# Kernel optimization log

Measured on AMD Instinct MI355X. Metric: run time of the kernel, lower is better.

## Reference

```python
import jax, jax.numpy as jnp
import numpy as np

D_MODEL = 2048
D_STATE = 128
D_CONV = 4
NHEADS = 64
NGROUPS = 1
HEAD_DIM = 64
CHUNK = 128
EPS = 1e-5
D_INNER = NHEADS * HEAD_DIM                       # 4096
CONV_DIM = D_INNER + 2 * NGROUPS * D_STATE        # 4352
D_IN_PROJ = 2 * D_INNER + 2 * NGROUPS * D_STATE + NHEADS  # 8512


def setup_inputs() -> dict:
    key = jax.random.key(0)
    ks = jax.random.split(key, 9)
    B, S = 2, 4096
    return dict(
        hidden_states=jax.random.normal(ks[0], (B, S, D_MODEL), jnp.float32),
        W_in=jax.random.normal(ks[1], (D_MODEL, D_IN_PROJ), jnp.float32) * 0.02,
        conv_w=jax.random.normal(ks[2], (CONV_DIM, D_CONV), jnp.float32) * 0.2,
        conv_b=jax.random.normal(ks[3], (CONV_DIM,), jnp.float32) * 0.1,
        # A must be negative (stable SSM): A = -exp(u), u ~ U[0,2)
        A=-jnp.exp(jax.random.uniform(ks[4], (NHEADS,), jnp.float32, 0.0, 2.0)),
        D=jax.random.normal(ks[5], (NHEADS,), jnp.float32),
        dt_bias=jax.random.normal(ks[6], (NHEADS,), jnp.float32),
        norm_w=jnp.ones((D_INNER,), jnp.float32),
        W_out=jax.random.normal(ks[7], (D_INNER, D_MODEL), jnp.float32) * 0.02,
    )


def _silu(x):
    return x * jax.nn.sigmoid(x)


def _causal_conv1d(x, w, b):
    # depthwise causal conv with silu; x [B,S,C], w [C,K], b [C]
    K = w.shape[1]
    S = x.shape[1]
    xp = jnp.pad(x, ((0, 0), (K - 1, 0), (0, 0)))
    y = sum(xp[:, k:k + S, :] * w[None, None, :, k].swapaxes(-1, -1) for k in range(0))
    y = jnp.zeros_like(x)
    for k in range(K):
        y = y + xp[:, k:k + S, :] * w[:, k][None, None, :]
    return _silu(y + b)


def _ssd(x, dt, A, Bm, Cm, chunk):
    # Mamba2 chunked SSD scan.
    # x [b,s,h,p]; dt [b,s,h] (>0); A [h]; Bm,Cm [b,s,g,n]
    b, s, h, p = x.shape
    g, n = Bm.shape[2], Bm.shape[3]
    hh = h // g
    c = s // chunk
    x = x.reshape(b, c, chunk, g, hh, p)
    dt = dt.reshape(b, c, chunk, g, hh)
    Bm = Bm.reshape(b, c, chunk, g, n)
    Cm = Cm.reshape(b, c, chunk, g, n)
    dA = dt * A.reshape(g, hh)                 # [b,c,l,g,hh]
    dA_cs = jnp.cumsum(dA, axis=2)             # [b,c,l,g,hh]
    dtx = dt[..., None] * x                    # [b,c,l,g,hh,p]
    # intra-chunk (diagonal blocks): L[i,j] = exp(sum_{j<k<=i} dA)
    diff = dA_cs[:, :, :, None] - dA_cs[:, :, None, :]   # [b,c,i,j,g,hh]
    mask = jnp.tril(jnp.ones((chunk, chunk), bool))
    L = jnp.exp(jnp.where(mask[None, None, :, :, None, None], diff, -jnp.inf))
    Y = jnp.einsum('bcign,bcjgn,bcijgh,bcjghp->bcighp', Cm, Bm, L, dtx)
    # chunk-final states
    decay = jnp.exp(dA_cs[:, :, -1:] - dA_cs)            # [b,c,l,g,hh]
    states = jnp.einsum('bcjgn,bcjgh,bcjghp->bcghpn', Bm, decay, dtx)
    chunk_decay = jnp.exp(dA_cs[:, :, -1])               # [b,c,g,hh]
    def step(prev, inp):
        cd, st = inp
        return cd[..., None, None] * prev + st, prev
    init = jnp.zeros_like(states[:, 0])
    _, prevs = jax.lax.scan(step, init,
                            (jnp.moveaxis(chunk_decay, 1, 0), jnp.moveaxis(states, 1, 0)))
    prevs = jnp.moveaxis(prevs, 0, 1)                    # [b,c,g,hh,p,n] state entering each chunk
    Y = Y + jnp.einsum('bcign,bcghpn,bcigh->bcighp', Cm, prevs, jnp.exp(dA_cs))
    return Y.reshape(b, s, h, p)


def reference(hidden_states, W_in, conv_w, conv_b, A, D, dt_bias, norm_w, W_out):
    Bsz, S, _ = hidden_states.shape
    zxbcdt = hidden_states @ W_in                        # [B,S,d_in_proj]
    z = zxbcdt[..., :D_INNER]
    xbc = zxbcdt[..., D_INNER:D_INNER + CONV_DIM]
    dt = zxbcdt[..., D_INNER + CONV_DIM:]                # [B,S,nheads]
    xbc = _causal_conv1d(xbc, conv_w, conv_b)            # silu-activated causal conv
    x = xbc[..., :D_INNER].reshape(Bsz, S, NHEADS, HEAD_DIM)
    Bm = xbc[..., D_INNER:D_INNER + NGROUPS * D_STATE].reshape(Bsz, S, NGROUPS, D_STATE)
    Cm = xbc[..., D_INNER + NGROUPS * D_STATE:].reshape(Bsz, S, NGROUPS, D_STATE)
    dt = jax.nn.softplus(dt + dt_bias)                   # delta_softplus, dt_limit=(0,inf)
    y = _ssd(x, dt, A, Bm, Cm, CHUNK)
    y = y + D[None, None, :, None] * x                   # skip (D) term
    y = y.reshape(Bsz, S, D_INNER)
    # gated RMSNorm (norm_before_gate=False): normalize(y * silu(z)), grouped
    yg = y * _silu(z)
    gsz = D_INNER // NGROUPS
    ygr = yg.reshape(Bsz, S, NGROUPS, gsz)
    rms = jax.lax.rsqrt(jnp.mean(ygr * ygr, axis=-1, keepdims=True) + EPS)
    yn = (ygr * rms).reshape(Bsz, S, D_INNER) * norm_w
    return yn @ W_out
```

## Files before the change

kernel.cpp:

```cpp
#include <hip/hip_runtime.h>
#include <hip/hip_bf16.h>

typedef __bf16 bf16_t;
typedef bf16_t bf16x8 __attribute__((ext_vector_type(8)));
typedef float f32x4 __attribute__((ext_vector_type(4)));

#define TOK 8192
#define DMODEL 2048
#define DINNER 4096
#define XBCN 4352
#define DSTATE 128
#define NH 64
#define HD 64
#define NBC 64
#define WINT_ROWS 8448

__device__ __forceinline__ void gld16(const bf16_t* g, bf16_t* l) {
  __builtin_amdgcn_global_load_lds((const __attribute__((address_space(1))) void*)g,
                                   (__attribute__((address_space(3))) void*)l, 16, 0, 0);
}

__device__ __forceinline__ f32x4 mfma16(bf16x8 a, bf16x8 b, f32x4 c) {
  return __builtin_amdgcn_mfma_f32_16x16x32_bf16(a, b, c, 0, 0, 0);
}


__global__ __launch_bounds__(256)
void cast_split_kernel(const float* __restrict__ in, bf16_t* __restrict__ hi,
                       bf16_t* __restrict__ lo, size_t n) {
  size_t i = ((size_t)blockIdx.x * 256 + threadIdx.x) * 8;
  if (i + 8 > n) return;
  float4 a = *(const float4*)(in + i);
  float4 b = *(const float4*)(in + i + 4);
  float v[8] = {a.x,a.y,a.z,a.w,b.x,b.y,b.z,b.w};
  bf16x8 h, l;
#pragma unroll
  for (int j = 0; j < 8; ++j) {
    h[j] = (bf16_t)v[j];
    l[j] = (bf16_t)(v[j] - (float)h[j]);
  }
  *(bf16x8*)(hi + i) = h;
  *(bf16x8*)(lo + i) = l;
}

__global__ __launch_bounds__(256)
void transpose_cast_kernel(const float* __restrict__ in, bf16_t* __restrict__ out,
                           int R, int C, int outRows) {
  __shared__ float tile[32][33];
  const int c0 = blockIdx.x * 32;
  const int r0 = blockIdx.y * 32;
  const int tx = threadIdx.x & 31;
  const int ty = threadIdx.x >> 5;
#pragma unroll
  for (int k = 0; k < 4; ++k) {
    int r = r0 + ty + k*8;
    int c = c0 + tx;
    tile[ty + k*8][tx] = (c < C) ? in[(size_t)r * C + c] : 0.f;
  }
  __syncthreads();
#pragma unroll
  for (int k = 0; k < 4; ++k) {
    int oc = c0 + ty + k*8;
    int orr = r0 + tx;
    out[(size_t)oc * R + orr] = (bf16_t)tile[tx][ty + k*8];
  }
}

__global__ __launch_bounds__(256)
void wdt_split_kernel(const float* __restrict__ Win, bf16_t* __restrict__ Whi,
                      bf16_t* __restrict__ Wlo) {
  const int h = threadIdx.x & 63;
  const int k0 = blockIdx.x * 256 + (threadIdx.x >> 6) * 64;
#pragma unroll 4
  for (int i = 0; i < 64; ++i) {
    int k = k0 + i;
    float v = Win[(size_t)k * 8512 + 8448 + h];
    bf16_t hv = (bf16_t)v;
    Whi[(size_t)h * DMODEL + k] = hv;
    Wlo[(size_t)h * DMODEL + k] = (bf16_t)(v - (float)hv);
  }
}

template <typename OutT>
__global__ __launch_bounds__(512, 2)
void gemm256(const bf16_t* __restrict__ A, const bf16_t* __restrict__ B,
             OutT* __restrict__ C0, OutT* __restrict__ C1,
             long M, long N, long K, long splitN, int gridX) {
  __shared__ bf16_t sA[2][2][8192];
  __shared__ bf16_t sB[2][2][8192];
  const int tid = threadIdx.x;
  const int lane = tid & 63;
  const int wid = tid >> 6;
  const int wr = wid >> 2;
  const int wc = wid & 3;

  const int nwg = gridDim.x;
  const int cpx = nwg >> 3;
  const int swz = (blockIdx.x & 7) * cpx + (blockIdx.x >> 3);
  const long bm = (long)(swz / gridX) * 256;
  const long bn = (long)(swz % gridX) * 256;

  const int srow = (wid >> 1) * 16 + (lane & 15);
  const int skof = (wid & 1) * 32 + (lane >> 4) * 8;
  const bf16_t* Abase = A + (bm + srow) * K + skof;
  const bf16_t* Bbase = B + (bn + srow) * K + skof;

  auto stageA = [&](int buf, int h, long kt) {
    const bf16_t* s = Abase + (long)h * 128 * K + kt;
    gld16(s,          &sA[buf][h][wid * 512]);
    gld16(s + 64 * K, &sA[buf][h][4096 + wid * 512]);
  };
  auto stageB = [&](int buf, int h, long kt) {
    const bf16_t* s = Bbase + (long)h * 128 * K + kt;
    gld16(s,          &sB[buf][h][wid * 512]);
    gld16(s + 64 * K, &sB[buf][h][4096 + wid * 512]);
  };
  auto rdA = [&](int buf, int h, int f, int s) -> bf16x8 {
    return *(const bf16x8*)&sA[buf][h][((f * 2 + s) * 64 + lane) * 8];
  };
  auto rdB = [&](int buf, int h, int f, int s) -> bf16x8 {
    return *(const bf16x8*)&sB[buf][h][((f * 2 + s) * 64 + lane) * 8];
  };

  stageA(0, 0, 0); stageB(0, 0, 0); stageB(0, 1, 0); stageA(0, 1, 0);

  f32x4 acc[8][4] = {};
  bf16x8 a[4][2], b[2][2];
  int cur = 0;
  const int NT = (int)(K >> 6);

  for (int t = 0; t < NT; ++t) {
    const bool fin = (t == NT - 1);
    const long ktn = (long)(t + 1) * 64;
    asm volatile("s_waitcnt vmcnt(4)\n\ts_barrier" ::: "memory");
#pragma unroll
    for (int mi = 0; mi < 4; ++mi) {
      a[mi][0] = rdA(cur, 0, wr*4 + mi, 0);
      a[mi][1] = rdA(cur, 0, wr*4 + mi, 1);
    }
#pragma unroll
    for (int ni = 0; ni < 2; ++ni) {
      b[ni][0] = rdB(cur, 0, wc*2 + ni, 0);
      b[ni][1] = rdB(cur, 0, wc*2 + ni, 1);
    }
    if (!fin) stageA(cur ^ 1, 0, ktn);
    __builtin_amdgcn_s_setprio(1);
#pragma unroll
    for (int mi = 0; mi < 4; ++mi)
#pragma unroll
      for (int ni = 0; ni < 2; ++ni) {
        acc[mi][ni] = mfma16(a[mi][0], b[ni][0], acc[mi][ni]);
        acc[mi][ni] = mfma16(a[mi][1], b[ni][1], acc[mi][ni]);
      }
    __builtin_amdgcn_s_setprio(0);
    if (!fin) asm volatile("s_waitcnt vmcnt(4)\n\ts_barrier" ::: "memory");
    else      asm volatile("s_waitcnt vmcnt(2)\n\ts_barrier" ::: "memory");
#pragma unroll
    for (int ni = 0; ni < 2; ++ni) {
      b[ni][0] = rdB(cur, 1, wc*2 + ni, 0);
      b[ni][1] = rdB(cur, 1, wc*2 + ni, 1);
    }
    if (!fin) stageB(cur ^ 1, 0, ktn);
    __builtin_amdgcn_s_setprio(1);
#pragma unroll
    for (int mi = 0; mi < 4; ++mi)
#pragma unroll
      for (int ni = 0; ni < 2; ++ni) {
        acc[mi][2 + ni] = mfma16(a[mi][0], b[ni][0], acc[mi][2 + ni]);
        acc[mi][2 + ni] = mfma16(a[mi][1], b[ni][1], acc[mi][2 + ni]);
      }
    __builtin_amdgcn_s_setprio(0);
    if (!fin) asm volatile("s_waitcnt vmcnt(4)\n\ts_barrier" ::: "memory");
    else      asm volatile("s_waitcnt vmcnt(0)\n\ts_barrier" ::: "memory");
#pragma unroll
    for (int mi = 0; mi < 4; ++mi) {
      a[mi][0] = rdA(cur, 1, wr*4 + mi, 0);
      a[mi][1] = rdA(cur, 1, wr*4 + mi, 1);
    }
    if (!fin) stageB(cur ^ 1, 1, ktn);
    __builtin_amdgcn_s_setprio(1);
#pragma unroll
    for (int mi = 0; mi < 4; ++mi)
#pragma unroll
      for (int ni = 0; ni < 2; ++ni) {
        acc[4 + mi][2 + ni] = mfma16(a[mi][0], b[ni][0], acc[4 + mi][2 + ni]);
        acc[4 + mi][2 + ni] = mfma16(a[mi][1], b[ni][1], acc[4 + mi][2 + ni]);
      }
    __builtin_amdgcn_s_setprio(0);
    asm volatile("s_barrier" ::: "memory");
#pragma unroll
    for (int ni = 0; ni < 2; ++ni) {
      b[ni][0] = rdB(cur, 0, wc*2 + ni, 0);
      b[ni][1] = rdB(cur, 0, wc*2 + ni, 1);
    }
    if (!fin) stageA(cur ^ 1, 1, ktn);
    __builtin_amdgcn_s_setprio(1);
#pragma unroll
    for (int mi = 0; mi < 4; ++mi)
#pragma unroll
      for (int ni = 0; ni < 2; ++ni) {
        acc[4 + mi][ni] = mfma16(a[mi][0], b[ni][0], acc[4 + mi][ni]);
        acc[4 + mi][ni] = mfma16(a[mi][1], b[ni][1], acc[4 + mi][ni]);
      }
    __builtin_amdgcn_s_setprio(0);
    cur ^= 1;
  }

  const int cr = (lane >> 4) * 4;
  const int cc = lane & 15;
  OutT* Cb;
  long col0, ldc;
  if (bn < splitN) { Cb = C0; col0 = bn; ldc = splitN; }
  else             { Cb = C1; col0 = bn - splitN; ldc = N - splitN; }
#pragma unroll
  for (int mi = 0; mi < 8; ++mi) {
    long row = bm + (mi >> 2) * 128 + wr * 64 + (mi & 3) * 16 + cr;
#pragma unroll
    for (int ni = 0; ni < 4; ++ni) {
      long col = col0 + (ni >> 1) * 128 + wc * 32 + (ni & 1) * 16 + cc;
      OutT* p = Cb + row * ldc + col;
#pragma unroll
      for (int r = 0; r < 4; ++r) p[(long)r * ldc] = (OutT)acc[mi][ni][r];
    }
  }
}

__global__ __launch_bounds__(256)
void dt_mfma_kernel(const bf16_t* __restrict__ Ahi, const bf16_t* __restrict__ Alo,
                    const bf16_t* __restrict__ Whi, const bf16_t* __restrict__ Wlo,
                    float* __restrict__ dtraw) {
  __shared__ bf16_t sAh[4096], sAl[4096], sBh[2048], sBl[2048];
  const int tid = threadIdx.x;
  const int lane = tid & 63;
  const int w = tid >> 6;
  const long bm = (long)blockIdx.x * 128;
  const int rlo = lane & 15;
  const int kq = lane >> 4;

  const bf16_t* Ah0 = Ahi + (bm + 2*w*16 + rlo) * (long)DMODEL + kq*8;
  const bf16_t* Ah1 = Ah0 + 16*(long)DMODEL;
  const bf16_t* Al0 = Alo + (bm + 2*w*16 + rlo) * (long)DMODEL + kq*8;
  const bf16_t* Al1 = Al0 + 16*(long)DMODEL;
  const bf16_t* Bh0 = Whi + (w*16 + rlo) * (long)DMODEL + kq*8;
  const bf16_t* Bl0 = Wlo + (w*16 + rlo) * (long)DMODEL + kq*8;

  f32x4 acc[2][4] = {};

  for (int kt = 0; kt < DMODEL; kt += 32) {
    __syncthreads();
    gld16(Ah0 + kt, &sAh[(2*w)*512]);
    gld16(Ah1 + kt, &sAh[(2*w+1)*512]);
    gld16(Al0 + kt, &sAl[(2*w)*512]);
    gld16(Al1 + kt, &sAl[(2*w+1)*512]);
    gld16(Bh0 + kt, &sBh[w*512]);
    gld16(Bl0 + kt, &sBl[w*512]);
    __syncthreads();
    bf16x8 ah[2], al[2], bh[4], bl[4];
#pragma unroll
    for (int i = 0; i < 2; ++i) {
      ah[i] = *(const bf16x8*)&sAh[((2*w + i)*64 + lane)*8];
      al[i] = *(const bf16x8*)&sAl[((2*w + i)*64 + lane)*8];
    }
#pragma unroll
    for (int n = 0; n < 4; ++n) {
      bh[n] = *(const bf16x8*)&sBh[(n*64 + lane)*8];
      bl[n] = *(const bf16x8*)&sBl[(n*64 + lane)*8];
    }
#pragma unroll
    for (int mi = 0; mi < 2; ++mi)
#pragma unroll
      for (int n = 0; n < 4; ++n) {
        acc[mi][n] = mfma16(ah[mi], bh[n], acc[mi][n]);
        acc[mi][n] = mfma16(ah[mi], bl[n], acc[mi][n]);
        acc[mi][n] = mfma16(al[mi], bh[n], acc[mi][n]);
      }
  }

  const int cr = (lane >> 4) * 4;
  const int cc = lane & 15;
#pragma unroll
  for (int mi = 0; mi < 2; ++mi)
#pragma unroll
    for (int n = 0; n < 4; ++n)
#pragma unroll
      for (int r = 0; r < 4; ++r)
        dtraw[(bm + 2*w*16 + mi*16 + cr + r) * 64 + n*16 + cc] = acc[mi][n][r];
}

__global__ __launch_bounds__(256)
void conv_kernel(const bf16_t* __restrict__ xbc, const float* __restrict__ cw,
                 const float* __restrict__ cb, bf16_t* __restrict__ xo,
                 bf16_t* __restrict__ Bout, bf16_t* __restrict__ Cout) {
  const int c = blockIdx.x * 256 + threadIdx.x;
  const int t0 = blockIdx.y * 8;
  const int bstart = (t0 >> 12) << 12;
  const float w0 = cw[c*4+0], w1 = cw[c*4+1], w2 = cw[c*4+2], w3 = cw[c*4+3];
  const float bias = cb[c];
  float in[11];
#pragma unroll
  for (int k = 0; k < 11; ++k) {
    int t = t0 - 3 + k;
    in[k] = (t >= bstart) ? (float)xbc[(size_t)t * XBCN + c] : 0.f;
  }
#pragma unroll
  for (int i = 0; i < 8; ++i) {
    float v = bias + w0*in[i] + w1*in[i+1] + w2*in[i+2] + w3*in[i+3];
    float s = v / (1.f + __expf(-v));
    int t = t0 + i;
    bf16_t o = (bf16_t)s;
    if (c < DINNER)           xo[(size_t)t * DINNER + c] = o;
    else if (c < DINNER+128)  Bout[(size_t)t * DSTATE + (c - DINNER)] = o;
    else                      Cout[(size_t)t * DSTATE + (c - DINNER - 128)] = o;
  }
}

__global__ __launch_bounds__(256)
void dt_scan_kernel(const float* __restrict__ dtraw, const float* __restrict__ dt_bias,
                    const float* __restrict__ Avec, float* __restrict__ dt_s,
                    float* __restrict__ dAcs, float* __restrict__ cdec) {
  const int wid = blockIdx.x * 4 + (threadIdx.x >> 6);
  const int lane = threadIdx.x & 63;
  const int h = wid & 63;
  const int bc = wid >> 6;
  const long tok0 = (long)bc * 128;
  const float Ah = Avec[h];
  const float bias = dt_bias[h];
  float v0 = dtraw[(tok0 + lane)*64 + h] + bias;
  float v1 = dtraw[(tok0 + 64 + lane)*64 + h] + bias;
  float d0 = (v0 > 20.f) ? v0 : log1pf(expf(v0));
  float d1 = (v1 > 20.f) ? v1 : log1pf(expf(v1));
  float s0 = d0 * Ah;
  float s1 = d1 * Ah;
#pragma unroll
  for (int off = 1; off < 64; off <<= 1) {
    float t = __shfl_up(s0, off);
    if (lane >= off) s0 += t;
  }
  float tot0 = __shfl(s0, 63);
#pragma unroll
  for (int off = 1; off < 64; off <<= 1) {
    float t = __shfl_up(s1, off);
    if (lane >= off) s1 += t;
  }
  s1 += tot0;
  const size_t base = (size_t)wid * 128;
  dt_s[base + lane] = d0;
  dt_s[base + 64 + lane] = d1;
  dAcs[base + lane] = s0;
  dAcs[base + 64 + lane] = s1;
  if (lane == 63) cdec[wid] = __expf(s1);
}

__global__ __launch_bounds__(256)
void states_kernel(const bf16_t* __restrict__ x, const bf16_t* __restrict__ Bm,
                   const float* __restrict__ dt_s, const float* __restrict__ dAcs,
                   bf16_t* __restrict__ states) {
  __shared__ bf16_t sDtx[8192];
  __shared__ bf16_t sBd[16384];
  __shared__ float sDt[128];
  __shared__ float sDec[128];
  const int wid = blockIdx.x;
  const int h = wid & 63;
  const int bc = wid >> 6;
  const int tid = threadIdx.x;
  const int lane = tid & 63;
  const int w = tid >> 6;
  const long tok0 = (long)bc * 128;
  const size_t dbase = (size_t)wid * 128;

  if (tid < 128) {
    sDt[tid] = dt_s[dbase + tid];
  } else {
    int j = tid - 128;
    sDec[j] = __expf(dAcs[dbase + 127] - dAcs[dbase + j]);
  }
  __syncthreads();

  {
    const int jj0 = tid >> 3;
    const int pg = (tid & 7) * 8;
#pragma unroll
    for (int t = 0; t < 4; ++t) {
      int j = t*32 + jj0;
      bf16x8 xv = *(const bf16x8*)&x[(tok0 + j)*(long)DINNER + h*64 + pg];
      float dtj = sDt[j];
      int kq = (j >> 5) * 4;
      int qe = ((j >> 3) & 3) * 16;
      int e = j & 7;
#pragma unroll
      for (int i = 0; i < 8; ++i) {
        int p = pg + i;
        sDtx[((kq + (p>>4))*64 + qe + (p&15))*8 + e] = (bf16_t)((float)xv[i]*dtj);
      }
    }
    const int jj1 = tid >> 4;
    const int ng = (tid & 15) * 8;
#pragma unroll
    for (int t = 0; t < 8; ++t) {
      int j = t*16 + jj1;
      bf16x8 bv = *(const bf16x8*)&Bm[(tok0 + j)*(long)DSTATE + ng];
      float dec = sDec[j];
      int kq = (j >> 5) * 8;
      int qe = ((j >> 3) & 3) * 16;
      int e = j & 7;
#pragma unroll
      for (int i = 0; i < 8; ++i) {
        int n = ng + i;
        sBd[((kq + (n>>4))*64 + qe + (n&15))*8 + e] = (bf16_t)((float)bv[i]*dec);
      }
    }
  }
  __syncthreads();

  f32x4 acc[4][2] = {};
#pragma unroll
  for (int kt = 0; kt < 4; ++kt) {
    bf16x8 aF[4], bF[2];
#pragma unroll
    for (int mt = 0; mt < 4; ++mt) aF[mt] = *(const bf16x8*)&sDtx[((kt*4 + mt)*64 + lane)*8];
#pragma unroll
    for (int nt = 0; nt < 2; ++nt) bF[nt] = *(const bf16x8*)&sBd[((kt*8 + w*2 + nt)*64 + lane)*8];
#pragma unroll
    for (int mt = 0; mt < 4; ++mt)
#pragma unroll
      for (int nt = 0; nt < 2; ++nt)
        acc[mt][nt] = mfma16(aF[mt], bF[nt], acc[mt][nt]);
  }

  bf16_t* S = states + (size_t)wid * (HD * DSTATE);
  const int cr = (lane >> 4) * 4;
  const int cc = lane & 15;
#pragma unroll
  for (int mt = 0; mt < 4; ++mt)
#pragma unroll
    for (int nt = 0; nt < 2; ++nt) {
      int n = (w*2 + nt)*16 + cc;
#pragma unroll
      for (int r = 0; r < 4; ++r) {
        int p = mt*16 + cr + r;
        S[(size_t)p*DSTATE + n] = (bf16_t)acc[mt][nt][r];
      }
    }
}

__global__ __launch_bounds__(256)
void scan_kernel(bf16_t* __restrict__ sp, const float* __restrict__ cdec) {
  const size_t gid = (size_t)blockIdx.x * 256 + threadIdx.x;
  const int n = gid & 127;
  const int p = (gid >> 7) & 63;
  const int h = (gid >> 13) & 63;
  const int b = (int)(gid >> 19);
  float prev = 0.f;
  const size_t pn = (size_t)p * 128 + n;
  for (int c = 0; c < 32; ++c) {
    const int wid = (b*32 + c)*64 + h;
    const size_t idx = (size_t)wid * 8192 + pn;
    float s = (float)sp[idx];
    sp[idx] = (bf16_t)prev;
    prev = cdec[wid] * prev + s;
  }
}

__global__ __launch_bounds__(256)
void ssd_y_kernel(bf16_t* __restrict__ xy, const bf16_t* __restrict__ Bm,
                  const bf16_t* __restrict__ Cm, const bf16_t* __restrict__ prevs,
                  const float* __restrict__ dt_s, const float* __restrict__ dAcs,
                  const float* __restrict__ Dvec) {
  __shared__ bf16_t sG[16384];
  __shared__ bf16_t sDtx[8192];
  __shared__ float sDA[128];
  __shared__ float sEA[128];
  __shared__ float sDt[128];

  const int wid = blockIdx.x;
  const int h = wid & 63;
  const int bc = wid >> 6;
  const int tid = threadIdx.x;
  const int lane = tid & 63;
  const int w = tid >> 6;
  const long tok0 = (long)bc * 128;
  const size_t dbase = (size_t)wid * 128;

  if (tid < 128) {
    float v = dAcs[dbase + tid];
    sDA[tid] = v;
    sEA[tid] = __expf(v);
  } else {
    sDt[tid - 128] = dt_s[dbase + tid - 128];
  }
  __syncthreads();

  {
    const int jj0 = tid >> 3;
    const int pg = (tid & 7) * 8;
#pragma unroll
    for (int t = 0; t < 4; ++t) {
      int j = t*32 + jj0;
      bf16x8 xv = *(const bf16x8*)&xy[(tok0 + j)*(long)DINNER + h*64 + pg];
      float dtj = sDt[j];
      int kq = (j >> 5) * 4;
      int qe = ((j >> 3) & 3) * 16;
      int e = j & 7;
#pragma unroll
      for (int i = 0; i < 8; ++i) {
        int p = pg + i;
        sDtx[((kq + (p>>4))*64 + qe + (p&15))*8 + e] = (bf16_t)((float)xv[i]*dtj);
      }
    }
  }

  const int arow = (w*2)*16 + (lane & 15);
  const int koff = (lane >> 4) * 8;
  bf16x8 aCm[2][4];
#pragma unroll
  for (int mi = 0; mi < 2; ++mi)
#pragma unroll
    for (int kt = 0; kt < 4; ++kt)
      aCm[mi][kt] = *(const bf16x8*)&Cm[(tok0 + arow + mi*16)*(long)DSTATE + kt*32 + koff];

  const bf16_t* P = prevs + (size_t)wid * 8192;
  f32x4 accY[2][4] = {};
#pragma unroll
  for (int kt = 0; kt < 4; ++kt) {
    bf16x8 bP[4];
#pragma unroll
    for (int ni = 0; ni < 4; ++ni)
      bP[ni] = *(const bf16x8*)&P[(size_t)(ni*16 + (lane & 15))*DSTATE + kt*32 + koff];
#pragma unroll
    for (int mi = 0; mi < 2; ++mi)
#pragma unroll
      for (int ni = 0; ni < 4; ++ni)
        accY[mi][ni] = mfma16(aCm[mi][kt], bP[ni], accY[mi][ni]);
  }
  const int cr = (lane >> 4) * 4;
  const int cc = lane & 15;
#pragma unroll
  for (int mi = 0; mi < 2; ++mi)
#pragma unroll
    for (int r = 0; r < 4; ++r) {
      float e = sEA[(w*2 + mi)*16 + cr + r];
#pragma unroll
      for (int ni = 0; ni < 4; ++ni) accY[mi][ni][r] *= e;
    }

  f32x4 accS[2][8] = {};
#pragma unroll
  for (int kt = 0; kt < 4; ++kt) {
    bf16x8 bB[8];
#pragma unroll
    for (int nt = 0; nt < 8; ++nt)
      bB[nt] = *(const bf16x8*)&Bm[(tok0 + nt*16 + (lane & 15))*(long)DSTATE + kt*32 + koff];
#pragma unroll
    for (int mi = 0; mi < 2; ++mi)
#pragma unroll
      for (int nt = 0; nt < 8; ++nt)
        accS[mi][nt] = mfma16(aCm[mi][kt], bB[nt], accS[mi][nt]);
  }

#pragma unroll
  for (int mi = 0; mi < 2; ++mi)
#pragma unroll
    for (int nt = 0; nt < 8; ++nt)
#pragma unroll
      for (int r = 0; r < 4; ++r) {
        int i = (w*2 + mi)*16 + cr + r;
        int j = nt*16 + cc;
        float g = (i >= j) ? accS[mi][nt][r] * __expf(sDA[i] - sDA[j]) : 0.f;
        sG[(((j>>5)*8 + (i>>4))*64 + ((j>>3)&3)*16 + (i&15))*8 + (j&7)] = (bf16_t)g;
      }
  __syncthreads();

#pragma unroll
  for (int kt = 0; kt < 4; ++kt) {
    bf16x8 aG[2], bD[4];
#pragma unroll
    for (int mi = 0; mi < 2; ++mi) aG[mi] = *(const bf16x8*)&sG[((kt*8 + w*2 + mi)*64 + lane)*8];
#pragma unroll
    for (int ni = 0; ni < 4; ++ni) bD[ni] = *(const bf16x8*)&sDtx[((kt*4 + ni)*64 + lane)*8];
#pragma unroll
    for (int mi = 0; mi < 2; ++mi)
#pragma unroll
      for (int ni = 0; ni < 4; ++ni)
        accY[mi][ni] = mfma16(aG[mi], bD[ni], accY[mi][ni]);
  }

  const float Dh = Dvec[h];
#pragma unroll
  for (int mi = 0; mi < 2; ++mi)
#pragma unroll
    for (int ni = 0; ni < 4; ++ni)
#pragma unroll
      for (int r = 0; r < 4; ++r) {
        long tokr = tok0 + (w*2 + mi)*16 + cr + r;
        int p = ni*16 + cc;
        long idx = tokr * DINNER + h*64 + p;
        float xv = (float)xy[idx];
        xy[idx] = (bf16_t)(accY[mi][ni][r] + Dh * xv);
      }
}

__global__ __launch_bounds__(256)
void gate_kernel(const bf16_t* __restrict__ y, const bf16_t* __restrict__ z,
                 const float* __restrict__ norm_w, bf16_t* __restrict__ yn) {
  const int tok = blockIdx.x;
  const int tid = threadIdx.x;
  const int lane = tid & 63;
  const int w = tid >> 6;
  const bf16_t* yrow = y + (size_t)tok * DINNER;
  const bf16_t* zrow = z + (size_t)tok * DINNER;
  float local[16];
  float ss = 0.f;
#pragma unroll
  for (int v = 0; v < 2; ++v) {
    int col = tid*16 + v*8;
    bf16x8 yv = *(const bf16x8*)&yrow[col];
    bf16x8 zv = *(const bf16x8*)&zrow[col];
#pragma unroll
    for (int i = 0; i < 8; ++i) {
      float zf = (float)zv[i];
      float g = zf / (1.f + __expf(-zf));
      float t = (float)yv[i] * g;
      local[v*8 + i] = t;
      ss += t*t;
    }
  }
#pragma unroll
  for (int off = 32; off > 0; off >>= 1) ss += __shfl_xor(ss, off);
  __shared__ float red[4];
  if (lane == 0) red[w] = ss;
  __syncthreads();
  float rms = rsqrtf((red[0]+red[1]+red[2]+red[3]) * (1.f/DINNER) + 1e-5f);
  bf16_t* orow = yn + (size_t)tok * DINNER;
#pragma unroll
  for (int v = 0; v < 2; ++v) {
    int col = tid*16 + v*8;
    bf16x8 o;
#pragma unroll
    for (int i = 0; i < 8; ++i) o[i] = (bf16_t)(local[v*8+i] * rms * norm_w[col+i]);
    *(bf16x8*)&orow[col] = o;
  }
}

extern "C" void kernel_launch(void* const* d_in, const int* in_sizes, int n_in,
                              void* d_out, int out_size, void* d_ws, size_t ws_size,
                              hipStream_t stream) {
  const float* hidden  = (const float*)d_in[0];
  const float* W_in    = (const float*)d_in[1];
  const float* conv_w  = (const float*)d_in[2];
  const float* conv_b  = (const float*)d_in[3];
  const float* Avec    = (const float*)d_in[4];
  const float* Dvec    = (const float*)d_in[5];
  const float* dt_bias = (const float*)d_in[6];
  const float* norm_w  = (const float*)d_in[7];
  const float* W_out   = (const float*)d_in[8];

  char* ws = (char*)d_ws;
  size_t off = 0;
  auto take = [&](size_t bytes) -> char* {
    char* p = ws + off;
    off += (bytes + 255) & ~(size_t)255;
    return p;
  };
  bf16_t* R1    = (bf16_t*)take((size_t)NBC * NH * HD * DSTATE * 2);
  bf16_t* WinT  = (bf16_t*)take((size_t)WINT_ROWS * DMODEL * 2);
  bf16_t* xbc   = (bf16_t*)take((size_t)TOK * XBCN * 2);
  bf16_t* xconv = (bf16_t*)take((size_t)TOK * DINNER * 2);
  bf16_t* Bmat  = (bf16_t*)take((size_t)TOK * DSTATE * 2);
  bf16_t* Cmat  = (bf16_t*)take((size_t)TOK * DSTATE * 2);
  float*  dtraw = (float*)take((size_t)TOK * NH * 4);
  float*  dt_s  = (float*)take((size_t)TOK * NH * 4);
  float*  dAcs  = (float*)take((size_t)TOK * NH * 4);
  float*  cdec  = (float*)take((size_t)NBC * NH * 4);
  bf16_t* Wdth  = (bf16_t*)take((size_t)NH * DMODEL * 2);
  bf16_t* Wdtl  = (bf16_t*)take((size_t)NH * DMODEL * 2);
  if (off > ws_size) return;

  bf16_t* Xb      = R1;
  bf16_t* Xlo     = xbc;
  bf16_t* statesB = R1;
  bf16_t* ynbuf   = R1;
  bf16_t* WoutT   = WinT;
  bf16_t* zbuf    = (bf16_t*)d_out;
  float*  out     = (float*)d_out;

  cast_split_kernel<<<(TOK*DMODEL)/2048, 256, 0, stream>>>(hidden, Xb, Xlo, (size_t)TOK*DMODEL);
  wdt_split_kernel<<<DMODEL/256, 256, 0, stream>>>(W_in, Wdth, Wdtl);
  dt_mfma_kernel<<<TOK/128, 256, 0, stream>>>(Xb, Xlo, Wdth, Wdtl, dtraw);
  transpose_cast_kernel<<<dim3(WINT_ROWS/32, DMODEL/32), 256, 0, stream>>>(W_in, WinT, DMODEL, 8512, WINT_ROWS);
  gemm256<bf16_t><<<(TOK/256)*(WINT_ROWS/256), 512, 0, stream>>>(
      Xb, WinT, zbuf, xbc, TOK, WINT_ROWS, DMODEL, DINNER, WINT_ROWS/256);
  transpose_cast_kernel<<<dim3(DMODEL/32, DINNER/32), 256, 0, stream>>>(W_out, WoutT, DINNER, DMODEL, DMODEL);
  conv_kernel<<<dim3(XBCN/256, TOK/8), 256, 0, stream>>>(xbc, conv_w, conv_b, xconv, Bmat, Cmat);
  dt_scan_kernel<<<(NBC*NH)/4, 256, 0, stream>>>(dtraw, dt_bias, Avec, dt_s, dAcs, cdec);
  states_kernel<<<NBC*NH, 256, 0, stream>>>(xconv, Bmat, dt_s, dAcs, statesB);
  scan_kernel<<<(NBC*NH*HD*DSTATE)/(32*256), 256, 0, stream>>>(statesB, cdec);
  ssd_y_kernel<<<NBC*NH, 256, 0, stream>>>(xconv, Bmat, Cmat, statesB, dt_s, dAcs, Dvec);
  gate_kernel<<<TOK, 256, 0, stream>>>(xconv, zbuf, norm_w, ynbuf);
  gemm256<float><<<(TOK/256)*(DMODEL/256), 512, 0, stream>>>(
      ynbuf, WoutT, out, out, TOK, DMODEL, DINNER, DMODEL, DMODEL/256);
}
```

Before: 1.090 ms.

## Hand-schedule GEMM LDS reads with inline asm and fixed block swizzle

Replaces compiler-generated LDS fragment reads with inline ds_read_b128 on precomputed base addresses, issues the next global-to-LDS stage before the LDS reads, and fences each MFMA phase with explicit lgkmcnt waits and sched_barriers. It also changes the workgroup-to-tile mapping to a fixed pattern that groups four M tiles per N column within each XCD slot. The goal is tighter control of instruction ordering and better L2 reuse, at the cost of hardcoding a grid shape assumption (gridX and splitN no longer drive the swizzle) and giving the compiler less freedom to interleave reads with math.

```diff
diff --git a/kernel.cpp b/kernel.cpp
--- a/kernel.cpp
+++ b/kernel.cpp
@@ -22,6 +22,12 @@
 
 __device__ __forceinline__ f32x4 mfma16(bf16x8 a, bf16x8 b, f32x4 c) {
   return __builtin_amdgcn_mfma_f32_16x16x32_bf16(a, b, c, 0, 0, 0);
+}
+
+__device__ __forceinline__ bf16x8 ldsr(unsigned addr) {
+  f32x4 r;
+  asm volatile("ds_read_b128 %0, %1" : "=v"(r) : "v"(addr));
+  return __builtin_bit_cast(bf16x8, r);
 }
 
 
@@ -94,11 +100,10 @@
   const int wr = wid >> 2;
   const int wc = wid & 3;
 
-  const int nwg = gridDim.x;
-  const int cpx = nwg >> 3;
-  const int swz = (blockIdx.x & 7) * cpx + (blockIdx.x >> 3);
-  const long bm = (long)(swz / gridX) * 256;
-  const long bn = (long)(swz % gridX) * 256;
+  const int x = blockIdx.x & 7;
+  const int q = blockIdx.x >> 3;
+  const long bm = (long)(x * 4 + (q & 3)) * 256;
+  const long bn = (long)(q >> 2) * 256;
 
   const int srow = (wid >> 1) * 16 + (lane & 15);
   const int skof = (wid & 1) * 32 + (lane >> 4) * 8;
@@ -115,12 +120,11 @@
     gld16(s,          &sB[buf][h][wid * 512]);
     gld16(s + 64 * K, &sB[buf][h][4096 + wid * 512]);
   };
-  auto rdA = [&](int buf, int h, int f, int s) -> bf16x8 {
-    return *(const bf16x8*)&sA[buf][h][((f * 2 + s) * 64 + lane) * 8];
-  };
-  auto rdB = [&](int buf, int h, int f, int s) -> bf16x8 {
-    return *(const bf16x8*)&sB[buf][h][((f * 2 + s) * 64 + lane) * 8];
-  };
+
+  const unsigned sAb = (unsigned)(uintptr_t)(__attribute__((address_space(3))) void*)&sA[0][0][0]
+                       + (unsigned)lane * 16 + (unsigned)wr * 8192;
+  const unsigned sBb = (unsigned)(uintptr_t)(__attribute__((address_space(3))) void*)&sB[0][0][0]
+                       + (unsigned)lane * 16 + (unsigned)wc * 4096;
 
   stageA(0, 0, 0); stageB(0, 0, 0); stageB(0, 1, 0); stageA(0, 1, 0);
 
@@ -132,18 +136,23 @@
   for (int t = 0; t < NT; ++t) {
     const bool fin = (t == NT - 1);
     const long ktn = (long)(t + 1) * 64;
+    const unsigned ab0 = sAb + (unsigned)cur * 32768;
+    const unsigned bb0 = sBb + (unsigned)cur * 32768;
+
     asm volatile("s_waitcnt vmcnt(4)\n\ts_barrier" ::: "memory");
+    if (!fin) stageA(cur ^ 1, 0, ktn);
 #pragma unroll
     for (int mi = 0; mi < 4; ++mi) {
-      a[mi][0] = rdA(cur, 0, wr*4 + mi, 0);
-      a[mi][1] = rdA(cur, 0, wr*4 + mi, 1);
+      a[mi][0] = ldsr(ab0 + (mi*2+0)*1024);
+      a[mi][1] = ldsr(ab0 + (mi*2+1)*1024);
     }
 #pragma unroll
     for (int ni = 0; ni < 2; ++ni) {
-      b[ni][0] = rdB(cur, 0, wc*2 + ni, 0);
-      b[ni][1] = rdB(cur, 0, wc*2 + ni, 1);
-    }
-    if (!fin) stageA(cur ^ 1, 0, ktn);
+      b[ni][0] = ldsr(bb0 + (ni*2+0)*1024);
+      b[ni][1] = ldsr(bb0 + (ni*2+1)*1024);
+    }
+    asm volatile("s_waitcnt lgkmcnt(0)" ::: "memory");
+    __builtin_amdgcn_sched_barrier(0);
     __builtin_amdgcn_s_setprio(1);
 #pragma unroll
     for (int mi = 0; mi < 4; ++mi)
@@ -153,14 +162,18 @@
         acc[mi][ni] = mfma16(a[mi][1], b[ni][1], acc[mi][ni]);
       }
     __builtin_amdgcn_s_setprio(0);
+    __builtin_amdgcn_sched_barrier(0);
+
     if (!fin) asm volatile("s_waitcnt vmcnt(4)\n\ts_barrier" ::: "memory");
     else      asm volatile("s_waitcnt vmcnt(2)\n\ts_barrier" ::: "memory");
+    if (!fin) stageB(cur ^ 1, 0, ktn);
 #pragma unroll
     for (int ni = 0; ni < 2; ++ni) {
-      b[ni][0] = rdB(cur, 1, wc*2 + ni, 0);
-      b[ni][1] = rdB(cur, 1, wc*2 + ni, 1);
-    }
-    if (!fin) stageB(cur ^ 1, 0, ktn);
+      b[ni][0] = ldsr(bb0 + 16384 + (ni*2+0)*1024);
+      b[ni][1] = ldsr(bb0 + 16384 + (ni*2+1)*1024);
+    }
+    asm volatile("s_waitcnt lgkmcnt(0)" ::: "memory");
+    __builtin_amdgcn_sched_barrier(0);
     __builtin_amdgcn_s_setprio(1);
 #pragma unroll
     for (int mi = 0; mi < 4; ++mi)
@@ -170,14 +183,18 @@
         acc[mi][2 + ni] = mfma16(a[mi][1], b[ni][1], acc[mi][2 + ni]);
       }
     __builtin_amdgcn_s_setprio(0);
+    __builtin_amdgcn_sched_barrier(0);
+
     if (!fin) asm volatile("s_waitcnt vmcnt(4)\n\ts_barrier" ::: "memory");
     else      asm volatile("s_waitcnt vmcnt(0)\n\ts_barrier" ::: "memory");
+    if (!fin) stageB(cur ^ 1, 1, ktn);
 #pragma unroll
     for (int mi = 0; mi < 4; ++mi) {
-      a[mi][0] = rdA(cur, 1, wr*4 + mi, 0);
-      a[mi][1] = rdA(cur, 1, wr*4 + mi, 1);
-    }
-    if (!fin) stageB(cur ^ 1, 1, ktn);
+      a[mi][0] = ldsr(ab0 + 16384 + (mi*2+0)*1024);
+      a[mi][1] = ldsr(ab0 + 16384 + (mi*2+1)*1024);
+    }
+    asm volatile("s_waitcnt lgkmcnt(0)" ::: "memory");
+    __builtin_amdgcn_sched_barrier(0);
     __builtin_amdgcn_s_setprio(1);
 #pragma unroll
     for (int mi = 0; mi < 4; ++mi)
@@ -187,13 +204,17 @@
         acc[4 + mi][2 + ni] = mfma16(a[mi][1], b[ni][1], acc[4 + mi][2 + ni]);
       }
     __builtin_amdgcn_s_setprio(0);
+    __builtin_amdgcn_sched_barrier(0);
+
     asm volatile("s_barrier" ::: "memory");
+    if (!fin) stageA(cur ^ 1, 1, ktn);
 #pragma unroll
     for (int ni = 0; ni < 2; ++ni) {
-      b[ni][0] = rdB(cur, 0, wc*2 + ni, 0);
-      b[ni][1] = rdB(cur, 0, wc*2 + ni, 1);
-    }
-    if (!fin) stageA(cur ^ 1, 1, ktn);
+      b[ni][0] = ldsr(bb0 + (ni*2+0)*1024);
+      b[ni][1] = ldsr(bb0 + (ni*2+1)*1024);
+    }
+    asm volatile("s_waitcnt lgkmcnt(0)" ::: "memory");
+    __builtin_amdgcn_sched_barrier(0);
     __builtin_amdgcn_s_setprio(1);
 #pragma unroll
     for (int mi = 0; mi < 4; ++mi)
@@ -203,6 +224,7 @@
         acc[4 + mi][ni] = mfma16(a[mi][1], b[ni][1], acc[4 + mi][ni]);
       }
     __builtin_amdgcn_s_setprio(0);
+    __builtin_amdgcn_sched_barrier(0);
     cur ^= 1;
   }
 
```

Measured after the change: 990.0 us. 1.1x faster.
